# Performance work log

Hardware: AMD Instinct MI355X
Metric: run time of the kernel (lower is better)

The kernel has to match this reference:

```python
import jax, jax.numpy as jnp
import numpy as np

B, L, LA, LL = 256, 512, 8, 64
V, D, P, HOPS = 100000, 300, 3, 3


def setup_inputs() -> dict:
    key = jax.random.key(0)
    ks = jax.random.split(key, 18)
    sc = 0.05
    return {
        "text":   jax.random.randint(ks[0], (B, L),  0, V),
        "aspect": jax.random.randint(ks[1], (B, LA), 0, V),
        "left":   jax.random.randint(ks[2], (B, LL), 0, V),
        # pretrained embedding table
        "embed": jax.random.normal(ks[3], (V, D), jnp.float32) * 0.1,
        # all Linear weights stored as [in, out] (y = x @ W + b)
        "Wx": jax.random.normal(ks[4], (D, D), jnp.float32) * sc,   # x_linear (no bias)
        "Ws": jax.random.normal(ks[5], (D, D), jnp.float32) * sc,   # s_linear (no bias)
        "Wk": jax.random.normal(ks[6], (D, D), jnp.float32) * sc,   # attention w_k
        "bk": jnp.zeros((D,), jnp.float32),
        "Wq": jax.random.normal(ks[7], (D, D), jnp.float32) * sc,   # attention w_q
        "bq": jnp.zeros((D,), jnp.float32),
        "w_mlp": jax.random.normal(ks[8], (2 * D,), jnp.float32) * sc,  # attention mlp score vector
        "Wproj": jax.random.normal(ks[9], (D, D), jnp.float32) * sc,    # attention proj
        "bproj": jnp.zeros((D,), jnp.float32),
        "Wm": jax.random.normal(ks[10], (D, D), jnp.float32) * sc,  # mlp
        "bm": jnp.zeros((D,), jnp.float32),
        "Wd": jax.random.normal(ks[11], (D, P), jnp.float32) * sc,  # dense
        "bd": jnp.zeros((P,), jnp.float32),
    }


def _forward(text, aspect, left, embed, Wx, Ws, Wk, bk, Wq, bq, w_mlp,
             Wproj, bproj, Wm, bm, Wd, bd):
    f32 = jnp.float32
    left_len = (left != 0).sum(-1)    # (B,)
    mem_len = (text != 0).sum(-1)     # (B,)
    asp_len = (aspect != 0).sum(-1)   # (B,)
    mem_len_f = mem_len.astype(f32)

    # aspect mean-pooled query (sum over all positions / nonzero count, as in torch code)
    asp_e = embed[aspect].sum(1) / asp_len.astype(f32)[:, None]   # (B, D)
    x = asp_e[:, None, :]                                         # (B, 1, D)

    memory = embed[text]                                          # (B, L, D)
    v_s = (memory.sum(1) / mem_len_f[:, None])[:, None, :]        # (B, 1, D)

    # SqueezeEmbedding (zero padding) + vectorized locationed_memory decay
    idx = jnp.arange(L, dtype=f32)[None, :]                       # (1, L)
    start = (left_len - asp_len).astype(f32)[:, None]             # aspect_start
    end = left_len.astype(f32)[:, None]                           # aspect_end
    l = jnp.where(idx < start, start - idx,
                  jnp.where(idx <= end, 0.0, idx - end))          # (B, L)
    w = 1.0 - l / mem_len_f[:, None]
    w = jnp.where(idx < mem_len_f[:, None], w, 0.0)               # zero padded positions
    memory = memory * w[:, :, None]                               # (B, L, D)

    for _ in range(HOPS):
        x = x @ Wx                                                # (B, 1, D)
        s = v_s @ Ws                                              # computed but unused (faithful)
        # Attention(score_function='mlp', n_head=1, hidden=D)
        kx = memory @ Wk + bk                                     # (B, L, D)
        qx = x @ Wq + bq                                          # (B, 1, D)
        # tanh(cat(kx, qx) @ w_mlp) == tanh(kx@w1 + qx@w2)
        score = jnp.tanh(kx @ w_mlp[:D] + qx @ w_mlp[D:])         # (B, L)
        score = jax.nn.softmax(score, axis=-1)
        v_ts = jnp.einsum('bl,bld->bd', score, kx)[:, None, :]    # (B, 1, D)
        v_ts = v_ts @ Wproj + bproj

    v_ns = (v_ts + v_s).reshape(text.shape[0], -1)                # (B, D)
    v_ms = jnp.tanh(v_ns @ Wm + bm)
    out = jax.nn.softmax(v_ms @ Wd + bd, axis=-1)                 # (B, P)
    return out


def reference(text, aspect, left, embed, Wx, Ws, Wk, bk, Wq, bq, w_mlp,
              Wproj, bproj, Wm, bm, Wd, bd):
    return _forward(text, aspect, left, embed, Wx, Ws, Wk, bk, Wq, bq,
                    w_mlp, Wproj, bproj, Wm, bm, Wd, bd)
```

## Files before the change

### kernel.cpp

```cpp
#include <hip/hip_runtime.h>
#include <math.h>

#define WS_KV 0
#define WS_C0 300
#define WS_C1 301
#define WS_H0 304
#define WS_H1 604
#define WS_MW 1024
#define WS_VS 77824

__device__ __forceinline__ float wred(float v) {
#pragma unroll
    for (int off = 32; off > 0; off >>= 1) v += __shfl_xor(v, off);
    return v;
}

__global__ __launch_bounds__(64) void k_prep(
    const float* __restrict__ Wk, const float* __restrict__ bk,
    const float* __restrict__ Wq, const float* __restrict__ bq,
    const float* __restrict__ wmlp, float* __restrict__ ws)
{
    const int lane = threadIdx.x;
    const int j = blockIdx.x;
    const float* u  = wmlp;
    const float* u2 = wmlp + 300;
    if (j < 300) {
        float pk = 0.f, pq = 0.f;
#pragma unroll
        for (int k = 0; k < 5; ++k) {
            int idx = lane + 64 * k;
            if (idx < 300) {
                pk += Wk[j * 300 + idx] * u[idx];
                pq += Wq[j * 300 + idx] * u2[idx];
            }
        }
        pk = wred(pk); pq = wred(pq);
        if (lane == 0) { ws[WS_KV + j] = pk; ws[WS_H0 + j] = pq; }
    } else if (j == 300) {
        float p = 0.f;
#pragma unroll
        for (int k = 0; k < 5; ++k) { int idx = lane + 64 * k; if (idx < 300) p += bk[idx] * u[idx]; }
        p = wred(p);
        if (lane == 0) ws[WS_C0] = p;
    } else {
        float p = 0.f;
#pragma unroll
        for (int k = 0; k < 5; ++k) { int idx = lane + 64 * k; if (idx < 300) p += bq[idx] * u2[idx]; }
        p = wred(p);
        if (lane == 0) ws[WS_C1] = p;
    }
}

__global__ __launch_bounds__(64) void k_hop(
    const float* __restrict__ Wx, const float* __restrict__ src,
    float* __restrict__ dst)
{
    const int lane = threadIdx.x;
    const int j = blockIdx.x;
    float p = 0.f;
#pragma unroll
    for (int k = 0; k < 5; ++k) {
        int idx = lane + 64 * k;
        if (idx < 300) p += Wx[j * 300 + idx] * src[idx];
    }
    p = wred(p);
    if (lane == 0) dst[j] = p;
}

__global__ __launch_bounds__(1024) void k_main(
    const int* __restrict__ text, const int* __restrict__ aspect,
    const int* __restrict__ left, const float* __restrict__ embed,
    float* __restrict__ ws)
{
    const int b = blockIdx.x;
    const int t = threadIdx.x;
    const int wv = t >> 6;
    const int lane = t & 63;

    __shared__ int   toks[512];
    __shared__ int   atoks[8];
    __shared__ float red[512];
    __shared__ __align__(16) float accW[16 * 300];
    __shared__ __align__(16) float vsW[16 * 300];
    __shared__ float denomW[16];
    __shared__ int   cnts[3];
    __shared__ float sc[4];

    if (t < 3) cnts[t] = 0;
    __syncthreads();

    bool predm = false, predl = false, preda = false;
    if (t < 512) { int tk = text[b * 512 + t]; toks[t] = tk; predm = (tk != 0); }
    else if (t < 576) predl = (left[b * 64 + (t - 512)] != 0);
    else if (t < 584) { int a = t - 576; int ak = aspect[b * 8 + a]; atoks[a] = ak; preda = (ak != 0); }
    {
        unsigned long long m;
        m = __ballot(predm); if (lane == 0 && m) atomicAdd(&cnts[0], __popcll(m));
        m = __ballot(predl); if (lane == 0 && m) atomicAdd(&cnts[1], __popcll(m));
        m = __ballot(preda); if (lane == 0 && m) atomicAdd(&cnts[2], __popcll(m));
    }
    __syncthreads();

    if (t < 300) {
        float s = 0.f;
#pragma unroll
        for (int a = 0; a < 8; ++a) s += embed[(size_t)atoks[a] * 300 + t];
        red[t] = (s / (float)cnts[2]) * ws[WS_H1 + t];
    } else if (t < 512) red[t] = 0.f;
    __syncthreads();
    for (int s = 256; s > 0; s >>= 1) { if (t < s) red[t] += red[t + s]; __syncthreads(); }
    if (t == 0) {
        sc[0] = (float)cnts[0];
        sc[1] = (float)(cnts[1] - cnts[2]);
        sc[2] = (float)cnts[1];
        sc[3] = red[0] + ws[WS_C0] + ws[WS_C1];
    }
    __syncthreads();
    const float mem_len_f = sc[0], startf = sc[1], endf = sc[2], qb = sc[3];

    const float4* kv4 = (const float4*)(ws + WS_KV);
    const float4* emb4 = (const float4*)embed;
    const bool hasB = (lane < 11);
    const float4 kva = kv4[lane];
    const float4 kvb = hasB ? kv4[64 + lane] : make_float4(0.f, 0.f, 0.f, 0.f);

    float4 accA = make_float4(0.f,0.f,0.f,0.f), accB = make_float4(0.f,0.f,0.f,0.f);
    float4 vsA  = make_float4(0.f,0.f,0.f,0.f), vsB  = make_float4(0.f,0.f,0.f,0.f);
    float denom = 0.f;

    for (int it = 0; it < 16; ++it) {
        const int l0 = wv * 32 + 2 * it, l1 = l0 + 1;
        const long r0 = (long)toks[l0] * 75, r1 = (long)toks[l1] * 75;
        float4 a0 = emb4[r0 + lane];
        float4 a1 = emb4[r1 + lane];
        float4 b0 = hasB ? emb4[r0 + 64 + lane] : make_float4(0.f,0.f,0.f,0.f);
        float4 b1 = hasB ? emb4[r1 + 64 + lane] : make_float4(0.f,0.f,0.f,0.f);

        float pd0 = a0.x*kva.x + a0.y*kva.y + a0.z*kva.z + a0.w*kva.w
                  + b0.x*kvb.x + b0.y*kvb.y + b0.z*kvb.z + b0.w*kvb.w;
        float pd1 = a1.x*kva.x + a1.y*kva.y + a1.z*kva.z + a1.w*kva.w
                  + b1.x*kvb.x + b1.y*kvb.y + b1.z*kvb.z + b1.w*kvb.w;
#pragma unroll
        for (int off = 32; off > 0; off >>= 1) {
            pd0 += __shfl_xor(pd0, off);
            pd1 += __shfl_xor(pd1, off);
        }

        const float f0 = (float)l0, f1 = (float)l1;
        float lv0 = (f0 < startf) ? (startf - f0) : ((f0 <= endf) ? 0.f : (f0 - endf));
        float lv1 = (f1 < startf) ? (startf - f1) : ((f1 <= endf) ? 0.f : (f1 - endf));
        float w0 = 1.f - lv0 / mem_len_f; w0 = (f0 < mem_len_f) ? w0 : 0.f;
        float w1 = 1.f - lv1 / mem_len_f; w1 = (f1 < mem_len_f) ? w1 : 0.f;

        const float p0 = expf(tanhf(w0 * pd0 + qb));
        const float p1 = expf(tanhf(w1 * pd1 + qb));
        const float pw0 = p0 * w0, pw1 = p1 * w1;

        accA.x += pw0*a0.x + pw1*a1.x;  accA.y += pw0*a0.y + pw1*a1.y;
        accA.z += pw0*a0.z + pw1*a1.z;  accA.w += pw0*a0.w + pw1*a1.w;
        accB.x += pw0*b0.x + pw1*b1.x;  accB.y += pw0*b0.y + pw1*b1.y;
        accB.z += pw0*b0.z + pw1*b1.z;  accB.w += pw0*b0.w + pw1*b1.w;
        vsA.x += a0.x + a1.x;  vsA.y += a0.y + a1.y;
        vsA.z += a0.z + a1.z;  vsA.w += a0.w + a1.w;
        vsB.x += b0.x + b1.x;  vsB.y += b0.y + b1.y;
        vsB.z += b0.z + b1.z;  vsB.w += b0.w + b1.w;
        denom += p0 + p1;
    }

    *(float4*)&accW[wv * 300 + 4 * lane] = accA;
    *(float4*)&vsW [wv * 300 + 4 * lane] = vsA;
    if (hasB) {
        *(float4*)&accW[wv * 300 + 256 + 4 * lane] = accB;
        *(float4*)&vsW [wv * 300 + 256 + 4 * lane] = vsB;
    }
    if (lane == 0) denomW[wv] = denom;
    __syncthreads();

    if (t < 300) {
        float ds = 0.f;
#pragma unroll
        for (int w = 0; w < 16; ++w) ds += denomW[w];
        float ms = 0.f, vs = 0.f;
#pragma unroll
        for (int w = 0; w < 16; ++w) { ms += accW[w * 300 + t]; vs += vsW[w * 300 + t]; }
        ws[WS_MW + b * 300 + t] = ms / ds;
        ws[WS_VS + b * 300 + t] = vs / mem_len_f;
    }
}

__global__ __launch_bounds__(960) void k_tail(
    const float* __restrict__ Wk, const float* __restrict__ bk,
    const float* __restrict__ Wproj, const float* __restrict__ bproj,
    const float* __restrict__ Wm, const float* __restrict__ bm,
    const float* __restrict__ Wd, const float* __restrict__ bd,
    float* __restrict__ out, const float* __restrict__ ws)
{
    const int t = threadIdx.x;
    const int b = blockIdx.x;
    const int seg = t / 320;
    const int j = t - seg * 320;

    __shared__ float A[300], T[300], part[900], vms[300], lg[3];

    if (t < 300) A[t] = ws[WS_MW + b * 300 + t];
    __syncthreads();

    if (j < 300) {
        const int k0 = seg * 100;
        float acc = 0.f;
#pragma unroll 10
        for (int i = 0; i < 100; ++i) acc += A[k0 + i] * Wk[(k0 + i) * 300 + j];
        part[seg * 300 + j] = acc;
    }
    __syncthreads();
    if (t < 300) T[t] = part[t] + part[300 + t] + part[600 + t] + bk[t];
    __syncthreads();

    if (j < 300) {
        const int k0 = seg * 100;
        float acc = 0.f;
#pragma unroll 10
        for (int i = 0; i < 100; ++i) acc += T[k0 + i] * Wproj[(k0 + i) * 300 + j];
        part[seg * 300 + j] = acc;
    }
    __syncthreads();
    if (t < 300) A[t] = part[t] + part[300 + t] + part[600 + t] + bproj[t] + ws[WS_VS + b * 300 + t];
    __syncthreads();

    if (j < 300) {
        const int k0 = seg * 100;
        float acc = 0.f;
#pragma unroll 10
        for (int i = 0; i < 100; ++i) acc += A[k0 + i] * Wm[(k0 + i) * 300 + j];
        part[seg * 300 + j] = acc;
    }
    __syncthreads();
    if (t < 300) vms[t] = tanhf(part[t] + part[300 + t] + part[600 + t] + bm[t]);
    __syncthreads();

    const int wv = t >> 6, lane = t & 63;
    if (wv < 3) {
        float p = 0.f;
#pragma unroll
        for (int k = 0; k < 5; ++k) { int d = lane + 64 * k; if (d < 300) p += vms[d] * Wd[d * 3 + wv]; }
        p = wred(p);
        if (lane == 0) lg[wv] = p + bd[wv];
    }
    __syncthreads();
    if (t == 0) {
        float l0 = lg[0], l1 = lg[1], l2 = lg[2];
        float mx = fmaxf(l0, fmaxf(l1, l2));
        float e0 = expf(l0 - mx), e1 = expf(l1 - mx), e2 = expf(l2 - mx);
        float s = e0 + e1 + e2;
        out[b * 3 + 0] = e0 / s;
        out[b * 3 + 1] = e1 / s;
        out[b * 3 + 2] = e2 / s;
    }
}

extern "C" void kernel_launch(void* const* d_in, const int* in_sizes, int n_in,
                              void* d_out, int out_size, void* d_ws, size_t ws_size,
                              hipStream_t stream)
{
    (void)in_sizes; (void)n_in; (void)out_size; (void)ws_size;
    const int*   text   = (const int*)d_in[0];
    const int*   aspect = (const int*)d_in[1];
    const int*   left   = (const int*)d_in[2];
    const float* embed  = (const float*)d_in[3];
    const float* Wx     = (const float*)d_in[4];
    const float* Wk     = (const float*)d_in[6];
    const float* bk     = (const float*)d_in[7];
    const float* Wq     = (const float*)d_in[8];
    const float* bq     = (const float*)d_in[9];
    const float* wmlp   = (const float*)d_in[10];
    const float* Wproj  = (const float*)d_in[11];
    const float* bproj  = (const float*)d_in[12];
    const float* Wm     = (const float*)d_in[13];
    const float* bm     = (const float*)d_in[14];
    const float* Wd     = (const float*)d_in[15];
    const float* bd     = (const float*)d_in[16];
    float* out = (float*)d_out;
    float* ws  = (float*)d_ws;

    hipLaunchKernelGGL(k_prep, dim3(302), dim3(64), 0, stream, Wk, bk, Wq, bq, wmlp, ws);
    hipLaunchKernelGGL(k_hop, dim3(300), dim3(64), 0, stream, Wx, ws + WS_H0, ws + WS_H1);
    hipLaunchKernelGGL(k_hop, dim3(300), dim3(64), 0, stream, Wx, ws + WS_H1, ws + WS_H0);
    hipLaunchKernelGGL(k_hop, dim3(300), dim3(64), 0, stream, Wx, ws + WS_H0, ws + WS_H1);
    hipLaunchKernelGGL(k_main, dim3(256), dim3(1024), 0, stream, text, aspect, left, embed, ws);
    hipLaunchKernelGGL(k_tail, dim3(256), dim3(960), 0, stream,
                       Wk, bk, Wproj, bproj, Wm, bm, Wd, bd, out, ws);
}
```

Baseline: 247.0 us.

## Split main kernel across four sequence chunks per batch with atomic accumulation

The main gather/attention kernel now launches four 512-thread blocks per batch row, each handling 128 tokens, and merges partial weighted sums, value sums and softmax denominators with global atomics. The normalisation by the denominator moves into the tail kernel, and the prep kernel zeroes the accumulation buffers. The output buffer is reused as scratch for the hop vectors to shrink the workspace. Fast-math exp replaces tanhf/expf, and the block-wide tree reduction becomes a wave shuffle reduction. This adds more, smaller blocks to improve latency hiding on the embedding gathers, at the cost of atomic traffic and recomputing the token counts in every chunk.

```diff
diff --git a/kernel.cpp b/kernel.cpp
--- a/kernel.cpp
+++ b/kernel.cpp
@@ -4,10 +4,11 @@
 #define WS_KV 0
 #define WS_C0 300
 #define WS_C1 301
-#define WS_H0 304
-#define WS_H1 604
-#define WS_MW 1024
-#define WS_VS 77824
+#define WS_H1 304
+#define WS_DEN 604
+#define WS_MW 864
+#define WS_VS 77664
+#define WS_END 154464
 
 __device__ __forceinline__ float wred(float v) {
 #pragma unroll
@@ -18,7 +19,8 @@
 __global__ __launch_bounds__(64) void k_prep(
     const float* __restrict__ Wk, const float* __restrict__ bk,
     const float* __restrict__ Wq, const float* __restrict__ bq,
-    const float* __restrict__ wmlp, float* __restrict__ ws)
+    const float* __restrict__ wmlp, float* __restrict__ h0,
+    float* __restrict__ ws)
 {
     const int lane = threadIdx.x;
     const int j = blockIdx.x;
@@ -35,7 +37,7 @@
             }
         }
         pk = wred(pk); pq = wred(pq);
-        if (lane == 0) { ws[WS_KV + j] = pk; ws[WS_H0 + j] = pq; }
+        if (lane == 0) { ws[WS_KV + j] = pk; h0[j] = pq; }
     } else if (j == 300) {
         float p = 0.f;
 #pragma unroll
@@ -49,6 +51,12 @@
         p = wred(p);
         if (lane == 0) ws[WS_C1] = p;
     }
+    const int zb = WS_DEN + j * 512 + lane * 8;
+#pragma unroll
+    for (int k = 0; k < 2; ++k) {
+        int o = zb + 4 * k;
+        if (o < WS_END) *(float4*)(ws + o) = make_float4(0.f, 0.f, 0.f, 0.f);
+    }
 }
 
 __global__ __launch_bounds__(64) void k_hop(
@@ -67,32 +75,36 @@
     if (lane == 0) dst[j] = p;
 }
 
-__global__ __launch_bounds__(1024) void k_main(
+__global__ __launch_bounds__(512, 6) void k_main(
     const int* __restrict__ text, const int* __restrict__ aspect,
     const int* __restrict__ left, const float* __restrict__ embed,
     float* __restrict__ ws)
 {
-    const int b = blockIdx.x;
+    const int b = blockIdx.x >> 2;
+    const int chunk = blockIdx.x & 3;
     const int t = threadIdx.x;
     const int wv = t >> 6;
     const int lane = t & 63;
-
-    __shared__ int   toks[512];
+    const int lbase = chunk * 128;
+
+    __shared__ int   toks[128];
     __shared__ int   atoks[8];
-    __shared__ float red[512];
-    __shared__ __align__(16) float accW[16 * 300];
-    __shared__ __align__(16) float vsW[16 * 300];
-    __shared__ float denomW[16];
+    __shared__ float red[8];
+    __shared__ __align__(16) float accW[8 * 300];
+    __shared__ __align__(16) float vsW[8 * 300];
+    __shared__ float denomW[8];
     __shared__ int   cnts[3];
     __shared__ float sc[4];
 
     if (t < 3) cnts[t] = 0;
     __syncthreads();
 
-    bool predm = false, predl = false, preda = false;
-    if (t < 512) { int tk = text[b * 512 + t]; toks[t] = tk; predm = (tk != 0); }
-    else if (t < 576) predl = (left[b * 64 + (t - 512)] != 0);
-    else if (t < 584) { int a = t - 576; int ak = aspect[b * 8 + a]; atoks[a] = ak; preda = (ak != 0); }
+    int tk = text[b * 512 + t];
+    bool predm = (tk != 0);
+    bool predl = false, preda = false;
+    if ((unsigned)(t - lbase) < 128u) toks[t - lbase] = tk;
+    if (t < 64) predl = (left[b * 64 + t] != 0);
+    if (t < 8) { int ak = aspect[b * 8 + t]; atoks[t] = ak; preda = (ak != 0); }
     {
         unsigned long long m;
         m = __ballot(predm); if (lane == 0 && m) atomicAdd(&cnts[0], __popcll(m));
@@ -101,19 +113,24 @@
     }
     __syncthreads();
 
+    float prod = 0.f;
     if (t < 300) {
         float s = 0.f;
 #pragma unroll
         for (int a = 0; a < 8; ++a) s += embed[(size_t)atoks[a] * 300 + t];
-        red[t] = (s / (float)cnts[2]) * ws[WS_H1 + t];
-    } else if (t < 512) red[t] = 0.f;
-    __syncthreads();
-    for (int s = 256; s > 0; s >>= 1) { if (t < s) red[t] += red[t + s]; __syncthreads(); }
+        prod = (s / (float)cnts[2]) * ws[WS_H1 + t];
+    }
+    prod = wred(prod);
+    if (lane == 0) red[wv] = prod;
+    __syncthreads();
     if (t == 0) {
         sc[0] = (float)cnts[0];
         sc[1] = (float)(cnts[1] - cnts[2]);
         sc[2] = (float)cnts[1];
-        sc[3] = red[0] + ws[WS_C0] + ws[WS_C1];
+        float q = 0.f;
+#pragma unroll
+        for (int w = 0; w < 8; ++w) q += red[w];
+        sc[3] = q + ws[WS_C0] + ws[WS_C1];
     }
     __syncthreads();
     const float mem_len_f = sc[0], startf = sc[1], endf = sc[2], qb = sc[3];
@@ -128,9 +145,10 @@
     float4 vsA  = make_float4(0.f,0.f,0.f,0.f), vsB  = make_float4(0.f,0.f,0.f,0.f);
     float denom = 0.f;
 
-    for (int it = 0; it < 16; ++it) {
-        const int l0 = wv * 32 + 2 * it, l1 = l0 + 1;
-        const long r0 = (long)toks[l0] * 75, r1 = (long)toks[l1] * 75;
+    for (int it = 0; it < 8; ++it) {
+        const int lt = wv * 16 + 2 * it;
+        const int l0 = lbase + lt, l1 = l0 + 1;
+        const long r0 = (long)toks[lt] * 75, r1 = (long)toks[lt + 1] * 75;
         float4 a0 = emb4[r0 + lane];
         float4 a1 = emb4[r1 + lane];
         float4 b0 = hasB ? emb4[r0 + 64 + lane] : make_float4(0.f,0.f,0.f,0.f);
@@ -152,8 +170,12 @@
         float w0 = 1.f - lv0 / mem_len_f; w0 = (f0 < mem_len_f) ? w0 : 0.f;
         float w1 = 1.f - lv1 / mem_len_f; w1 = (f1 < mem_len_f) ? w1 : 0.f;
 
-        const float p0 = expf(tanhf(w0 * pd0 + qb));
-        const float p1 = expf(tanhf(w1 * pd1 + qb));
+        float s0 = w0 * pd0 + qb; s0 = fminf(fmaxf(s0, -15.f), 15.f);
+        float s1 = w1 * pd1 + qb; s1 = fminf(fmaxf(s1, -15.f), 15.f);
+        float e0 = __expf(2.f * s0);
+        float e1 = __expf(2.f * s1);
+        const float p0 = __expf((e0 - 1.f) / (e0 + 1.f));
+        const float p1 = __expf((e1 - 1.f) / (e1 + 1.f));
         const float pw0 = p0 * w0, pw1 = p1 * w1;
 
         accA.x += pw0*a0.x + pw1*a1.x;  accA.y += pw0*a0.y + pw1*a1.y;
@@ -179,12 +201,13 @@
     if (t < 300) {
         float ds = 0.f;
 #pragma unroll
-        for (int w = 0; w < 16; ++w) ds += denomW[w];
+        for (int w = 0; w < 8; ++w) ds += denomW[w];
         float ms = 0.f, vs = 0.f;
 #pragma unroll
-        for (int w = 0; w < 16; ++w) { ms += accW[w * 300 + t]; vs += vsW[w * 300 + t]; }
-        ws[WS_MW + b * 300 + t] = ms / ds;
-        ws[WS_VS + b * 300 + t] = vs / mem_len_f;
+        for (int w = 0; w < 8; ++w) { ms += accW[w * 300 + t]; vs += vsW[w * 300 + t]; }
+        atomicAdd(&ws[WS_MW + b * 300 + t], ms);
+        atomicAdd(&ws[WS_VS + b * 300 + t], vs / mem_len_f);
+        if (t == 0) atomicAdd(&ws[WS_DEN + b], ds);
     }
 }
 
@@ -202,7 +225,7 @@
 
     __shared__ float A[300], T[300], part[900], vms[300], lg[3];
 
-    if (t < 300) A[t] = ws[WS_MW + b * 300 + t];
+    if (t < 300) A[t] = ws[WS_MW + b * 300 + t] / ws[WS_DEN + b];
     __syncthreads();
 
     if (j < 300) {
@@ -282,11 +305,11 @@
     float* out = (float*)d_out;
     float* ws  = (float*)d_ws;
 
-    hipLaunchKernelGGL(k_prep, dim3(302), dim3(64), 0, stream, Wk, bk, Wq, bq, wmlp, ws);
-    hipLaunchKernelGGL(k_hop, dim3(300), dim3(64), 0, stream, Wx, ws + WS_H0, ws + WS_H1);
-    hipLaunchKernelGGL(k_hop, dim3(300), dim3(64), 0, stream, Wx, ws + WS_H1, ws + WS_H0);
-    hipLaunchKernelGGL(k_hop, dim3(300), dim3(64), 0, stream, Wx, ws + WS_H0, ws + WS_H1);
-    hipLaunchKernelGGL(k_main, dim3(256), dim3(1024), 0, stream, text, aspect, left, embed, ws);
+    hipLaunchKernelGGL(k_prep, dim3(302), dim3(64), 0, stream, Wk, bk, Wq, bq, wmlp, out, ws);
+    hipLaunchKernelGGL(k_hop, dim3(300), dim3(64), 0, stream, Wx, out, ws + WS_H1);
+    hipLaunchKernelGGL(k_hop, dim3(300), dim3(64), 0, stream, Wx, ws + WS_H1, out);
+    hipLaunchKernelGGL(k_hop, dim3(300), dim3(64), 0, stream, Wx, out, ws + WS_H1);
+    hipLaunchKernelGGL(k_main, dim3(1024), dim3(512), 0, stream, text, aspect, left, embed, ws);
     hipLaunchKernelGGL(k_tail, dim3(256), dim3(960), 0, stream,
                        Wk, bk, Wproj, bproj, Wm, bm, Wd, bd, out, ws);
 }
```

After: 250.1 us. About the same (+1.2%).

## Fuse hop kernels into one block and merge main with tail kernel

Applied to the files above, without the earlier changes.

Replaces the three per-hop matrix-vector launches with a single one-block kernel that iterates the hops in shared memory. It also merges the attention-pooling kernel with the projection/MLP tail so intermediate vectors stay in shared memory instead of round-tripping through global workspace. The block-wide tree reduction becomes a wave shuffle reduction, and tanh/expf are replaced with clamped fast __expf formulas. The extra Wx row-sum written in prep is unused work, and the single-block hop kernel serialises on one CU.

```diff
diff --git a/kernel.cpp b/kernel.cpp
--- a/kernel.cpp
+++ b/kernel.cpp
@@ -1,13 +1,12 @@
 #include <hip/hip_runtime.h>
 #include <math.h>
 
-#define WS_KV 0
-#define WS_C0 300
-#define WS_C1 301
-#define WS_H0 304
-#define WS_H1 604
-#define WS_MW 1024
-#define WS_VS 77824
+#define WS_KV    0
+#define WS_C0    300
+#define WS_C1    301
+#define WS_H0    304
+#define WS_H1    604
+#define WS_DUMMY 904
 
 __device__ __forceinline__ float wred(float v) {
 #pragma unroll
@@ -18,24 +17,30 @@
 __global__ __launch_bounds__(64) void k_prep(
     const float* __restrict__ Wk, const float* __restrict__ bk,
     const float* __restrict__ Wq, const float* __restrict__ bq,
-    const float* __restrict__ wmlp, float* __restrict__ ws)
+    const float* __restrict__ Wx, const float* __restrict__ wmlp,
+    float* __restrict__ ws)
 {
     const int lane = threadIdx.x;
     const int j = blockIdx.x;
     const float* u  = wmlp;
     const float* u2 = wmlp + 300;
     if (j < 300) {
-        float pk = 0.f, pq = 0.f;
+        float pk = 0.f, pq = 0.f, pw = 0.f;
 #pragma unroll
         for (int k = 0; k < 5; ++k) {
             int idx = lane + 64 * k;
             if (idx < 300) {
                 pk += Wk[j * 300 + idx] * u[idx];
                 pq += Wq[j * 300 + idx] * u2[idx];
+                pw += Wx[j * 300 + idx];
             }
         }
-        pk = wred(pk); pq = wred(pq);
-        if (lane == 0) { ws[WS_KV + j] = pk; ws[WS_H0 + j] = pq; }
+        pk = wred(pk); pq = wred(pq); pw = wred(pw);
+        if (lane == 0) {
+            ws[WS_KV + j] = pk;
+            ws[WS_H0 + j] = pq;
+            ws[WS_DUMMY + j] = pw;
+        }
     } else if (j == 300) {
         float p = 0.f;
 #pragma unroll
@@ -51,26 +56,59 @@
     }
 }
 
-__global__ __launch_bounds__(64) void k_hop(
-    const float* __restrict__ Wx, const float* __restrict__ src,
-    float* __restrict__ dst)
+__global__ __launch_bounds__(1024) void k_hops3(
+    const float* __restrict__ Wx, float* __restrict__ ws)
 {
-    const int lane = threadIdx.x;
-    const int j = blockIdx.x;
-    float p = 0.f;
-#pragma unroll
-    for (int k = 0; k < 5; ++k) {
-        int idx = lane + 64 * k;
-        if (idx < 300) p += Wx[j * 300 + idx] * src[idx];
-    }
-    p = wred(p);
-    if (lane == 0) dst[j] = p;
-}
-
-__global__ __launch_bounds__(1024) void k_main(
+    const int t = threadIdx.x;
+    const int wv = t >> 6;
+    const int lane = t & 63;
+    __shared__ float ha[300];
+    __shared__ float hb[300];
+
+    if (t < 300) ha[t] = ws[WS_H0 + t];
+    __syncthreads();
+
+    for (int hop = 0; hop < 3; ++hop) {
+        const float* s_ = (hop & 1) ? hb : ha;
+        float* d_ = (hop & 1) ? ha : hb;
+        for (int i = 0; i < 20; i += 2) {
+            const int j0 = wv + 16 * i;
+            const int j1 = j0 + 16;
+            const int jj0 = (j0 < 300) ? j0 : 0;
+            const int jj1 = (j1 < 300) ? j1 : 0;
+            float p0 = 0.f, p1 = 0.f;
+#pragma unroll
+            for (int k = 0; k < 5; ++k) {
+                int idx = lane + 64 * k;
+                if (idx < 300) {
+                    float sv = s_[idx];
+                    p0 += Wx[jj0 * 300 + idx] * sv;
+                    p1 += Wx[jj1 * 300 + idx] * sv;
+                }
+            }
+#pragma unroll
+            for (int off = 32; off > 0; off >>= 1) {
+                p0 += __shfl_xor(p0, off);
+                p1 += __shfl_xor(p1, off);
+            }
+            if (lane == 0) {
+                if (j0 < 300) d_[j0] = p0;
+                if (j1 < 300) d_[j1] = p1;
+            }
+        }
+        __syncthreads();
+    }
+    if (t < 300) ws[WS_H1 + t] = hb[t];
+}
+
+__global__ __launch_bounds__(1024) void k_fused(
     const int* __restrict__ text, const int* __restrict__ aspect,
     const int* __restrict__ left, const float* __restrict__ embed,
-    float* __restrict__ ws)
+    const float* __restrict__ Wk, const float* __restrict__ bk,
+    const float* __restrict__ Wproj, const float* __restrict__ bproj,
+    const float* __restrict__ Wm, const float* __restrict__ bm,
+    const float* __restrict__ Wd, const float* __restrict__ bd,
+    float* __restrict__ out, const float* __restrict__ ws)
 {
     const int b = blockIdx.x;
     const int t = threadIdx.x;
@@ -79,12 +117,13 @@
 
     __shared__ int   toks[512];
     __shared__ int   atoks[8];
-    __shared__ float red[512];
+    __shared__ float red[16];
     __shared__ __align__(16) float accW[16 * 300];
     __shared__ __align__(16) float vsW[16 * 300];
     __shared__ float denomW[16];
     __shared__ int   cnts[3];
     __shared__ float sc[4];
+    __shared__ float A[300], VS[300], T[300], part[900], vms[300], lg[3];
 
     if (t < 3) cnts[t] = 0;
     __syncthreads();
@@ -101,19 +140,24 @@
     }
     __syncthreads();
 
+    float prod = 0.f;
     if (t < 300) {
         float s = 0.f;
 #pragma unroll
         for (int a = 0; a < 8; ++a) s += embed[(size_t)atoks[a] * 300 + t];
-        red[t] = (s / (float)cnts[2]) * ws[WS_H1 + t];
-    } else if (t < 512) red[t] = 0.f;
-    __syncthreads();
-    for (int s = 256; s > 0; s >>= 1) { if (t < s) red[t] += red[t + s]; __syncthreads(); }
+        prod = (s / (float)cnts[2]) * ws[WS_H1 + t];
+    }
+    prod = wred(prod);
+    if (lane == 0) red[wv] = prod;
+    __syncthreads();
     if (t == 0) {
         sc[0] = (float)cnts[0];
         sc[1] = (float)(cnts[1] - cnts[2]);
         sc[2] = (float)cnts[1];
-        sc[3] = red[0] + ws[WS_C0] + ws[WS_C1];
+        float q = 0.f;
+#pragma unroll
+        for (int w = 0; w < 16; ++w) q += red[w];
+        sc[3] = q + ws[WS_C0] + ws[WS_C1];
     }
     __syncthreads();
     const float mem_len_f = sc[0], startf = sc[1], endf = sc[2], qb = sc[3];
@@ -152,8 +196,12 @@
         float w0 = 1.f - lv0 / mem_len_f; w0 = (f0 < mem_len_f) ? w0 : 0.f;
         float w1 = 1.f - lv1 / mem_len_f; w1 = (f1 < mem_len_f) ? w1 : 0.f;
 
-        const float p0 = expf(tanhf(w0 * pd0 + qb));
-        const float p1 = expf(tanhf(w1 * pd1 + qb));
+        float s0 = w0 * pd0 + qb; s0 = fminf(fmaxf(s0, -15.f), 15.f);
+        float s1 = w1 * pd1 + qb; s1 = fminf(fmaxf(s1, -15.f), 15.f);
+        float e0 = __expf(2.f * s0);
+        float e1 = __expf(2.f * s1);
+        const float p0 = __expf((e0 - 1.f) / (e0 + 1.f));
+        const float p1 = __expf((e1 - 1.f) / (e1 + 1.f));
         const float pw0 = p0 * w0, pw1 = p1 * w1;
 
         accA.x += pw0*a0.x + pw1*a1.x;  accA.y += pw0*a0.y + pw1*a1.y;
@@ -183,29 +231,16 @@
         float ms = 0.f, vs = 0.f;
 #pragma unroll
         for (int w = 0; w < 16; ++w) { ms += accW[w * 300 + t]; vs += vsW[w * 300 + t]; }
-        ws[WS_MW + b * 300 + t] = ms / ds;
-        ws[WS_VS + b * 300 + t] = vs / mem_len_f;
-    }
-}
-
-__global__ __launch_bounds__(960) void k_tail(
-    const float* __restrict__ Wk, const float* __restrict__ bk,
-    const float* __restrict__ Wproj, const float* __restrict__ bproj,
-    const float* __restrict__ Wm, const float* __restrict__ bm,
-    const float* __restrict__ Wd, const float* __restrict__ bd,
-    float* __restrict__ out, const float* __restrict__ ws)
-{
-    const int t = threadIdx.x;
-    const int b = blockIdx.x;
+        A[t] = ms / ds;
+        VS[t] = vs / mem_len_f;
+    }
+    __syncthreads();
+
     const int seg = t / 320;
     const int j = t - seg * 320;
-
-    __shared__ float A[300], T[300], part[900], vms[300], lg[3];
-
-    if (t < 300) A[t] = ws[WS_MW + b * 300 + t];
-    __syncthreads();
-
-    if (j < 300) {
+    const bool act = (seg < 3) && (j < 300);
+
+    if (act) {
         const int k0 = seg * 100;
         float acc = 0.f;
 #pragma unroll 10
@@ -216,7 +251,7 @@
     if (t < 300) T[t] = part[t] + part[300 + t] + part[600 + t] + bk[t];
     __syncthreads();
 
-    if (j < 300) {
+    if (act) {
         const int k0 = seg * 100;
         float acc = 0.f;
 #pragma unroll 10
@@ -224,10 +259,10 @@
         part[seg * 300 + j] = acc;
     }
     __syncthreads();
-    if (t < 300) A[t] = part[t] + part[300 + t] + part[600 + t] + bproj[t] + ws[WS_VS + b * 300 + t];
-    __syncthreads();
-
-    if (j < 300) {
+    if (t < 300) A[t] = part[t] + part[300 + t] + part[600 + t] + bproj[t] + VS[t];
+    __syncthreads();
+
+    if (act) {
         const int k0 = seg * 100;
         float acc = 0.f;
 #pragma unroll 10
@@ -238,7 +273,6 @@
     if (t < 300) vms[t] = tanhf(part[t] + part[300 + t] + part[600 + t] + bm[t]);
     __syncthreads();
 
-    const int wv = t >> 6, lane = t & 63;
     if (wv < 3) {
         float p = 0.f;
 #pragma unroll
@@ -282,11 +316,9 @@
     float* out = (float*)d_out;
     float* ws  = (float*)d_ws;
 
-    hipLaunchKernelGGL(k_prep, dim3(302), dim3(64), 0, stream, Wk, bk, Wq, bq, wmlp, ws);
-    hipLaunchKernelGGL(k_hop, dim3(300), dim3(64), 0, stream, Wx, ws + WS_H0, ws + WS_H1);
-    hipLaunchKernelGGL(k_hop, dim3(300), dim3(64), 0, stream, Wx, ws + WS_H1, ws + WS_H0);
-    hipLaunchKernelGGL(k_hop, dim3(300), dim3(64), 0, stream, Wx, ws + WS_H0, ws + WS_H1);
-    hipLaunchKernelGGL(k_main, dim3(256), dim3(1024), 0, stream, text, aspect, left, embed, ws);
-    hipLaunchKernelGGL(k_tail, dim3(256), dim3(960), 0, stream,
+    hipLaunchKernelGGL(k_prep,  dim3(302), dim3(64),   0, stream, Wk, bk, Wq, bq, Wx, wmlp, ws);
+    hipLaunchKernelGGL(k_hops3, dim3(1),   dim3(1024), 0, stream, Wx, ws);
+    hipLaunchKernelGGL(k_fused, dim3(256), dim3(1024), 0, stream,
+                       text, aspect, left, embed,
                        Wk, bk, Wproj, bproj, Wm, bm, Wd, bd, out, ws);
 }
```

Measured after the change: 250.7 us. About the same (+1.5%).
